# Kernel optimization log

Measured on AMD Instinct MI355X. Metric: run time of the kernel, lower is better.

Reference implementation:

```python
import jax, jax.numpy as jnp
import numpy as np
import itertools

K = 3   # kernel_size
G = 24  # octahedral rotation group order (reflection=False)

def _octa_tables(k):
    # 24 proper rotations of the cube as signed permutation matrices (det=+1)
    mats = []
    for perm in itertools.permutations(range(3)):
        for signs in itertools.product((1, -1), repeat=3):
            M = np.zeros((3, 3), dtype=np.int64)
            for i in range(3):
                M[i, perm[i]] = signs[i]
            if int(round(np.linalg.det(M))) == 1:
                mats.append(M)
    idx = {m.tobytes(): i for i, m in enumerate(mats)}
    n = len(mats)
    # shifted_indices[g][h] = index of g^{-1} h  (g^{-1} = g.T for signed perms)
    shift = np.array([[idx[(mats[g].T @ mats[h]).tobytes()] for h in range(n)] for g in range(n)])
    # spatial rotation gather maps: out[c] = in[R^{-1} c] on a centered k^3 grid
    c = (k - 1) / 2.0
    coords = np.stack(np.meshgrid(*([np.arange(k)] * 3), indexing='ij'), -1).reshape(-1, 3)
    rot = []
    for m in mats:
        src = np.rint((coords - c) @ m + c).astype(np.int64)
        rot.append(src[:, 0] * k * k + src[:, 1] * k + src[:, 2])
    return np.array(shift), np.array(rot)

SHIFT, ROT = _octa_tables(K)  # (G,G), (G,K^3)

def _gconv(x, weight, relaxed_w, bias, pad):
    # weight: (n_basis, out, in, G, k, k, k); x: (B, in, G, D, H, W)
    n, o, i, g, k, _, _ = weight.shape
    B = x.shape[0]
    w = weight[:, :, :, jnp.asarray(SHIFT)]            # (n,o,i,G_g,G,k,k,k) gather group axis
    wf = w.reshape(n, o, i, g, g, k ** 3)
    rot = jnp.asarray(ROT)[None, None, None, :, None, :]
    wf = jnp.take_along_axis(wf, jnp.broadcast_to(rot, wf.shape), axis=-1)  # rotate spatial per g
    fb = wf.transpose(0, 1, 3, 2, 4, 5).reshape(n, o, g, i * g, k, k, k)
    cw = jnp.einsum('ng,nogi...->ogi...', relaxed_w, fb).reshape(o * g, i * g, k, k, k)
    x2 = x.reshape(B, i * g, *x.shape[-3:])
    out = jax.lax.conv_general_dilated(x2, cw, (1, 1, 1), [(pad, pad)] * 3,
                                       dimension_numbers=('NCDHW', 'OIDHW', 'NCDHW'))
    out = out + jnp.repeat(bias[:, 0], g)[None, :, None, None, None]
    return out.reshape(B, o, g, *out.shape[-3:])

def _block(x, w1, rw1, b1, w2, rw2, b2):
    p = (K - 1) // 2
    h = jax.nn.leaky_relu(_gconv(x, w1, rw1, b1, p))   # layer1 activation=True
    h = _gconv(h, w2, rw2, b2, p)                      # layer2 activation=False
    return jax.nn.leaky_relu(h + x)                    # residual + block activation

def setup_inputs():
    key = jax.random.key(0)
    ks = jax.random.split(key, 5)
    C, NB = 16, 2
    x = jax.random.normal(ks[0], (2, C, G, 32, 32, 32), jnp.float32)
    s = float(np.sqrt(6.0 / (C * G * K ** 3)))  # kaiming-uniform-like scale
    w1 = jax.random.uniform(ks[1], (NB, C, C, G, K, K, K), jnp.float32, -s, s)
    w2 = jax.random.uniform(ks[2], (NB, C, C, G, K, K, K), jnp.float32, -s, s)
    rw1 = jnp.ones((NB, G), jnp.float32)  # relaxed_weights init to ones, as in torch
    rw2 = jnp.ones((NB, G), jnp.float32)
    b1 = jax.random.normal(ks[3], (C, 1), jnp.float32)
    b2 = jax.random.normal(ks[4], (C, 1), jnp.float32)
    return dict(x=x, w1=w1, rw1=rw1, b1=b1, w2=w2, rw2=rw2, b2=b2)

def reference(x, w1, rw1, b1, w2, rw2, b2):
    return _block(x, w1, rw1, b1, w2, rw2, b2)
```

## Files before the change

### kernel.cpp

```cpp
#include <hip/hip_runtime.h>
#include <hip/hip_bf16.h>
#include <stdint.h>

typedef __bf16 bf16x8 __attribute__((ext_vector_type(8)));
typedef float  f32x4  __attribute__((ext_vector_type(4)));
typedef short  short8v __attribute__((ext_vector_type(8)));

__device__ __forceinline__ void gload16(const void* gp, void* lp) {
  __builtin_amdgcn_global_load_lds(
      reinterpret_cast<const __attribute__((address_space(1))) uint32_t*>(
          reinterpret_cast<uintptr_t>(gp)),
      reinterpret_cast<__attribute__((address_space(3))) uint32_t*>(
          (uintptr_t)(uint32_t)reinterpret_cast<uintptr_t>(lp)),
      16, 0, 0);
}

__global__ void build_tables(int* __restrict__ shift, int* __restrict__ rot) {
  int tid = blockIdx.x * blockDim.x + threadIdx.x;
  if (tid >= 576 + 648) return;
  const int perms[6][3] = {{0,1,2},{0,2,1},{1,0,2},{1,2,0},{2,0,1},{2,1,0}};
  const int psign[6] = {1,-1,-1,1,1,-1};
  int mats[24][3][3];
  int nm = 0;
  for (int pi = 0; pi < 6; ++pi)
    for (int sb = 0; sb < 8; ++sb) {
      int s0 = (sb&4)?-1:1, s1 = (sb&2)?-1:1, s2 = (sb&1)?-1:1;
      if (psign[pi]*s0*s1*s2 != 1) continue;
      int sg[3] = {s0,s1,s2};
      for (int i = 0; i < 3; ++i)
        for (int j = 0; j < 3; ++j)
          mats[nm][i][j] = (j == perms[pi][i]) ? sg[i] : 0;
      ++nm;
    }
  if (tid < 576) {
    int g = tid / 24, h = tid % 24;
    int P[3][3];
    for (int i = 0; i < 3; ++i)
      for (int j = 0; j < 3; ++j) {
        int v = 0;
        for (int k = 0; k < 3; ++k) v += mats[g][k][i]*mats[h][k][j];
        P[i][j] = v;
      }
    int id = -1;
    for (int m = 0; m < 24 && id < 0; ++m) {
      bool eq = true;
      for (int i = 0; i < 3; ++i)
        for (int j = 0; j < 3; ++j) eq = eq && (mats[m][i][j] == P[i][j]);
      if (eq) id = m;
    }
    shift[tid] = id;
  } else {
    int r = tid - 576;
    int g = r / 27, vox = r % 27;
    int z = vox / 9, y = (vox / 3) % 3, x = vox % 3;
    int v[3] = {z-1, y-1, x-1}, s[3];
    for (int j = 0; j < 3; ++j) {
      int a = 0;
      for (int i = 0; i < 3; ++i) a += v[i]*mats[g][i][j];
      s[j] = a + 1;
    }
    rot[g*27 + vox] = (s[0]*3 + s[1])*3 + s[2];
  }
}

__global__ void prep_weights(const float* __restrict__ w, const float* __restrict__ rw,
                             const int* __restrict__ shift, const int* __restrict__ rot,
                             __hip_bfloat16* __restrict__ cw) {
  int idx = blockIdx.x*256 + threadIdx.x;
  if (idx >= 384*27*384) return;
  int icf = idx % 384;
  int s   = (idx / 384) % 27;
  int oc  = idx / (384*27);
  int i = icf / 24, h = icf - i*24;
  int o = oc  / 24, g = oc  - o*24;
  int gg = shift[g*24 + h];
  int ss = rot[g*27 + s];
  float v = rw[g]      * w[((o*16 + i)*24 + gg)*27 + ss]
          + rw[24 + g] * w[(((16 + o)*16 + i)*24 + gg)*27 + ss];
  cw[idx] = __float2bfloat16(v);
}

__global__ void fill_xpad(const float* __restrict__ x, __hip_bfloat16* __restrict__ xp) {
  __shared__ __hip_bfloat16 tile[32][72];
  int t = threadIdx.x;
  int r = blockIdx.x;
  int cg = blockIdx.y;
  int b = r >> 10, zy = r & 1023, z = zy >> 5, y = zy & 31;
  const float* src = x + (((size_t)(b*384 + cg*64)) << 15) + zy*32;
#pragma unroll
  for (int p = 0; p < 2; ++p) {
    int chr = p*32 + (t >> 3), part = t & 7;
    float4 v = *(const float4*)(src + (((size_t)chr) << 15) + part*4);
    tile[part*4+0][chr] = __float2bfloat16(v.x);
    tile[part*4+1][chr] = __float2bfloat16(v.y);
    tile[part*4+2][chr] = __float2bfloat16(v.z);
    tile[part*4+3][chr] = __float2bfloat16(v.w);
  }
  __syncthreads();
  int pos = t >> 3, pc = t & 7;
  size_t vox = ((size_t)(b*34 + z + 1)*34 + (y + 1))*34 + (pos + 1);
  short8v val = *(const short8v*)&tile[pos][pc*8];
  *(short8v*)((short*)xp + vox*384 + cg*64 + pc*8) = val;
}

template <int MODE>
__global__ __launch_bounds__(256, 2) void gconv(
    const __hip_bfloat16* __restrict__ src,
    const __hip_bfloat16* __restrict__ cw,
    const float* __restrict__ bias,
    const float* __restrict__ resid,
    __hip_bfloat16* __restrict__ hout,
    float* __restrict__ out) {
  __shared__ __align__(16) char lds[65536];
  const int tid  = threadIdx.x;
  const int lane = tid & 63, wid = tid >> 6;
  const int lrow = lane & 15, lq = lane >> 4;
  const int wm = wid >> 1, wn = wid & 1;
  const int bid = blockIdx.x;
  const int swz = (bid & 7) * 192 + (bid >> 3);
  const int tm = swz / 3;
  const int tn = swz - tm * 3;
  const int ocb = tn * 128;
  const int pbase = tm * 128;
  const int b  = pbase >> 15;
  const int zy = (pbase & 32767) >> 5;
  const int z = zy >> 5, y0 = zy & 31;

  f32x4 acc[4][4] = {};

  const int sx = tid >> 3;
  const int slot_sw = ((tid & 7) ^ ((tid >> 3) & 7)) * 16;
  const char* srcB = (const char*)src;
  const char* cwB  = (const char*)cw;
  int gA[4], gB[4];
#pragma unroll
  for (int p = 0; p < 4; ++p)
    gA[p] = (((b*34 + z)*34 + (y0 + p))*34 + sx) * 768 + slot_sw;
#pragma unroll
  for (int p = 0; p < 4; ++p)
    gB[p] = (ocb + p*32 + sx) * 20736 + slot_sw;

  const int xr = lrow & 7;
  const int s0 = (lq ^ xr) * 16;
  const int s1 = ((4 | lq) ^ xr) * 16;
  const int arow0 = (wm*64 + lrow) * 128;
  const int brow0 = 16384 + (wn*64 + lrow) * 128;

#pragma unroll
  for (int p = 0; p < 4; ++p) gload16(srcB + gA[p], lds + p*4096 + tid*16);
#pragma unroll
  for (int p = 0; p < 4; ++p) gload16(cwB + gB[p], lds + 16384 + p*4096 + tid*16);
  __syncthreads();

  int sic = 1, skx = 0, sky = 0, skz = 0, sta = 0, stb = 0;

  for (int t = 0; t < 162; ++t) {
    const int cur = t & 1;
    if (t < 161) {
      char* D = lds + (cur ^ 1) * 32768;
      const int ta = sta + sic*128, tb = stb + sic*128;
#pragma unroll
      for (int p = 0; p < 4; ++p) gload16(srcB + gA[p] + ta, D + p*4096 + tid*16);
#pragma unroll
      for (int p = 0; p < 4; ++p) gload16(cwB + gB[p] + tb, D + 16384 + p*4096 + tid*16);
      if (++sic == 6) {
        sic = 0;
        if (++skx == 3) { skx = 0; if (++sky == 3) { sky = 0; ++skz; } }
        sta = (skz*1156 + sky*34 + skx) * 768;
        stb += 768;
      }
    }
    const char* Ab = lds + cur * 32768;
#pragma unroll
    for (int h = 0; h < 2; ++h) {
      const int sh = h ? s1 : s0;
      bf16x8 bfr[4];
#pragma unroll
      for (int ni = 0; ni < 4; ++ni)
        bfr[ni] = *(const bf16x8*)(Ab + brow0 + ni*2048 + sh);
      __builtin_amdgcn_s_setprio(1);
#pragma unroll
      for (int mi = 0; mi < 4; ++mi) {
        bf16x8 af = *(const bf16x8*)(Ab + arow0 + mi*2048 + sh);
#pragma unroll
        for (int ni = 0; ni < 4; ++ni)
          acc[mi][ni] = __builtin_amdgcn_mfma_f32_16x16x32_bf16(
              af, bfr[ni], acc[mi][ni], 0, 0, 0);
      }
      __builtin_amdgcn_s_setprio(0);
    }
    __syncthreads();
  }

  float bias_n[4];
  int oc_n[4];
#pragma unroll
  for (int ni = 0; ni < 4; ++ni) {
    int oc = ocb + wn*64 + ni*16 + lrow;
    oc_n[ni] = oc;
    bias_n[ni] = bias[oc / 24];
  }
  if (MODE == 0) {
    const int voxb = ((b*34 + z + 1)*34 + (y0 + 1))*34 + 1;
#pragma unroll
    for (int mi = 0; mi < 4; ++mi) {
#pragma unroll
      for (int e = 0; e < 4; ++e) {
        int rr = wm*64 + mi*16 + lq*4 + e;
        int vox = voxb + (rr >> 5)*34 + (rr & 31);
        __hip_bfloat16* dst = hout + (size_t)vox*384;
#pragma unroll
        for (int ni = 0; ni < 4; ++ni) {
          float v = acc[mi][ni][e] + bias_n[ni];
          v = v >= 0.f ? v : 0.01f*v;
          dst[oc_n[ni]] = __float2bfloat16(v);
        }
      }
    }
  } else {
    const int zyx0 = pbase & 32767;
#pragma unroll
    for (int mi = 0; mi < 4; ++mi) {
      int rrb = wm*64 + mi*16 + lq*4;
#pragma unroll
      for (int ni = 0; ni < 4; ++ni) {
        size_t ofs = (((size_t)(b*384 + oc_n[ni])) << 15) + zyx0 + rrb;
        float4 res = *(const float4*)(resid + ofs);
        float rv[4] = {res.x, res.y, res.z, res.w};
        float ov[4];
#pragma unroll
        for (int e = 0; e < 4; ++e) {
          float v = acc[mi][ni][e] + bias_n[ni] + rv[e];
          ov[e] = v >= 0.f ? v : 0.01f*v;
        }
        float4 o4 = make_float4(ov[0], ov[1], ov[2], ov[3]);
        *(float4*)(out + ofs) = o4;
      }
    }
  }
}

extern "C" void kernel_launch(void* const* d_in, const int* in_sizes, int n_in,
                              void* d_out, int out_size, void* d_ws, size_t ws_size,
                              hipStream_t stream) {
  const float* x   = (const float*)d_in[0];
  const float* w1  = (const float*)d_in[1];
  const float* rw1 = (const float*)d_in[2];
  const float* b1  = (const float*)d_in[3];
  const float* w2  = (const float*)d_in[4];
  const float* rw2 = (const float*)d_in[5];
  const float* b2  = (const float*)d_in[6];
  float* out = (float*)d_out;

  char* ws = (char*)d_ws;
  int* shiftT = (int*)ws;
  int* rotT   = (int*)(ws + 2304);
  const size_t CW_BYTES  = (size_t)384*27*384*2;
  const size_t PAD_BYTES = (size_t)2*34*34*34*384*2;
  __hip_bfloat16* cw1  = (__hip_bfloat16*)(ws + 8192);
  __hip_bfloat16* cw2  = (__hip_bfloat16*)(ws + 8192 + CW_BYTES);
  __hip_bfloat16* xpad = (__hip_bfloat16*)(ws + 8192 + 2*CW_BYTES);
  __hip_bfloat16* hpad = (__hip_bfloat16*)(ws + 8192 + 2*CW_BYTES + PAD_BYTES);

  hipMemsetAsync(xpad, 0, PAD_BYTES, stream);
  hipMemsetAsync(hpad, 0, PAD_BYTES, stream);
  build_tables<<<5, 256, 0, stream>>>(shiftT, rotT);
  prep_weights<<<(384*27*384 + 255)/256, 256, 0, stream>>>(w1, rw1, shiftT, rotT, cw1);
  prep_weights<<<(384*27*384 + 255)/256, 256, 0, stream>>>(w2, rw2, shiftT, rotT, cw2);
  fill_xpad<<<dim3(2048, 6), 256, 0, stream>>>(x, xpad);
  gconv<0><<<dim3(1536, 1), 256, 0, stream>>>(xpad, cw1, b1, nullptr, hpad, nullptr);
  gconv<1><<<dim3(1536, 1), 256, 0, stream>>>(hpad, cw2, b2, x, nullptr, out);
}
```

Baseline: 1.078 ms.

## Load weight fragments directly from global into registers, halving LDS buffer

The B operand (convolution weights) is no longer staged through LDS. Each thread now loads its own MFMA fragments straight from global memory into double-buffered registers, prefetched one iteration ahead, and the loop is unrolled by two to swap the register buffers. This cuts LDS use from 64KB to 32KB, which may allow more resident blocks, and removes the LDS write/read traffic for B. The cost is uncoalesced per-thread global loads, duplicated across the two wm waves, plus higher register pressure that may push against the launch bounds.

After: 2.266 ms. +110.2%, slower.

```diff
diff --git a/kernel.cpp b/kernel.cpp
--- a/kernel.cpp
+++ b/kernel.cpp
@@ -111,7 +111,7 @@
     const float* __restrict__ resid,
     __hip_bfloat16* __restrict__ hout,
     float* __restrict__ out) {
-  __shared__ __align__(16) char lds[65536];
+  __shared__ __align__(16) char lds[32768];
   const int tid  = threadIdx.x;
   const int lane = tid & 63, wid = tid >> 6;
   const int lrow = lane & 15, lq = lane >> 4;
@@ -132,65 +132,74 @@
   const int slot_sw = ((tid & 7) ^ ((tid >> 3) & 7)) * 16;
   const char* srcB = (const char*)src;
   const char* cwB  = (const char*)cw;
-  int gA[4], gB[4];
+  int gA[4];
 #pragma unroll
   for (int p = 0; p < 4; ++p)
     gA[p] = (((b*34 + z)*34 + (y0 + p))*34 + sx) * 768 + slot_sw;
-#pragma unroll
-  for (int p = 0; p < 4; ++p)
-    gB[p] = (ocb + p*32 + sx) * 20736 + slot_sw;
+
+  const char* cwTh = cwB + (ptrdiff_t)(ocb + wn*64 + lrow) * 20736 + lq*16;
 
   const int xr = lrow & 7;
   const int s0 = (lq ^ xr) * 16;
   const int s1 = ((4 | lq) ^ xr) * 16;
   const int arow0 = (wm*64 + lrow) * 128;
-  const int brow0 = 16384 + (wn*64 + lrow) * 128;
+
+  bf16x8 bA[4][2], bB[4][2];
 
 #pragma unroll
   for (int p = 0; p < 4; ++p) gload16(srcB + gA[p], lds + p*4096 + tid*16);
 #pragma unroll
-  for (int p = 0; p < 4; ++p) gload16(cwB + gB[p], lds + 16384 + p*4096 + tid*16);
+  for (int ni = 0; ni < 4; ++ni) {
+    bA[ni][0] = *(const bf16x8*)(cwTh + ni*331776);
+    bA[ni][1] = *(const bf16x8*)(cwTh + ni*331776 + 64);
+  }
   __syncthreads();
 
   int sic = 1, skx = 0, sky = 0, skz = 0, sta = 0, stb = 0;
 
-  for (int t = 0; t < 162; ++t) {
-    const int cur = t & 1;
-    if (t < 161) {
-      char* D = lds + (cur ^ 1) * 32768;
-      const int ta = sta + sic*128, tb = stb + sic*128;
-#pragma unroll
-      for (int p = 0; p < 4; ++p) gload16(srcB + gA[p] + ta, D + p*4096 + tid*16);
-#pragma unroll
-      for (int p = 0; p < 4; ++p) gload16(cwB + gB[p] + tb, D + 16384 + p*4096 + tid*16);
-      if (++sic == 6) {
-        sic = 0;
-        if (++skx == 3) { skx = 0; if (++sky == 3) { sky = 0; ++skz; } }
-        sta = (skz*1156 + sky*34 + skx) * 768;
-        stb += 768;
-      }
-    }
-    const char* Ab = lds + cur * 32768;
-#pragma unroll
-    for (int h = 0; h < 2; ++h) {
-      const int sh = h ? s1 : s0;
-      bf16x8 bfr[4];
-#pragma unroll
-      for (int ni = 0; ni < 4; ++ni)
-        bfr[ni] = *(const bf16x8*)(Ab + brow0 + ni*2048 + sh);
-      __builtin_amdgcn_s_setprio(1);
-#pragma unroll
-      for (int mi = 0; mi < 4; ++mi) {
-        bf16x8 af = *(const bf16x8*)(Ab + arow0 + mi*2048 + sh);
-#pragma unroll
-        for (int ni = 0; ni < 4; ++ni)
-          acc[mi][ni] = __builtin_amdgcn_mfma_f32_16x16x32_bf16(
-              af, bfr[ni], acc[mi][ni], 0, 0, 0);
-      }
-      __builtin_amdgcn_s_setprio(0);
-    }
-    __syncthreads();
-  }
+#define ITER(T, BCUR, BNXT) do {                                               \
+    const int cur = (T) & 1;                                                   \
+    if ((T) < 161) {                                                           \
+      char* D = lds + (cur ^ 1) * 16384;                                       \
+      const int ta = sta + sic*128, tb = stb + sic*128;                        \
+      _Pragma("unroll")                                                        \
+      for (int p = 0; p < 4; ++p)                                              \
+        gload16(srcB + gA[p] + ta, D + p*4096 + tid*16);                       \
+      _Pragma("unroll")                                                        \
+      for (int ni = 0; ni < 4; ++ni) {                                         \
+        BNXT[ni][0] = *(const bf16x8*)(cwTh + ni*331776 + tb);                 \
+        BNXT[ni][1] = *(const bf16x8*)(cwTh + ni*331776 + tb + 64);            \
+      }                                                                        \
+      if (++sic == 6) {                                                        \
+        sic = 0;                                                               \
+        if (++skx == 3) { skx = 0; if (++sky == 3) { sky = 0; ++skz; } }       \
+        sta = (skz*1156 + sky*34 + skx) * 768;                                 \
+        stb += 768;                                                            \
+      }                                                                        \
+    }                                                                          \
+    const char* Ab = lds + cur * 16384;                                        \
+    _Pragma("unroll")                                                          \
+    for (int h = 0; h < 2; ++h) {                                              \
+      const int sh = h ? s1 : s0;                                              \
+      __builtin_amdgcn_s_setprio(1);                                           \
+      _Pragma("unroll")                                                        \
+      for (int mi = 0; mi < 4; ++mi) {                                         \
+        bf16x8 af = *(const bf16x8*)(Ab + arow0 + mi*2048 + sh);               \
+        _Pragma("unroll")                                                      \
+        for (int ni = 0; ni < 4; ++ni)                                         \
+          acc[mi][ni] = __builtin_amdgcn_mfma_f32_16x16x32_bf16(               \
+              af, BCUR[ni][h], acc[mi][ni], 0, 0, 0);                          \
+      }                                                                        \
+      __builtin_amdgcn_s_setprio(0);                                           \
+    }                                                                          \
+    __syncthreads();                                                           \
+  } while (0)
+
+  for (int t = 0; t < 162; t += 2) {
+    ITER(t,     bA, bB);
+    ITER(t + 1, bB, bA);
+  }
+#undef ITER
 
   float bias_n[4];
   int oc_n[4];
```
